# Optimization experiments

Hardware: AMD Instinct MI355X
Metric: run time of the kernel (lower is better)

The kernel has to match this reference:

```python
import jax, jax.numpy as jnp
import numpy as np
import math

D_MODEL = 1024
N_HEADS = 16
HEAD_DIM = D_MODEL // N_HEADS

def setup_inputs() -> dict:
    key = jax.random.key(0)
    k1, k2, k3 = jax.random.split(key, 3)
    B, T = 4, 2048
    x = jax.random.normal(k1, (B, T, D_MODEL), dtype=jnp.float32)
    # weights stored as [in, out]; equivalent to torch Linear weight.T
    w_qkv = jax.random.normal(k2, (D_MODEL, 3 * D_MODEL), dtype=jnp.float32) * (1.0 / math.sqrt(D_MODEL))
    w_proj = jax.random.normal(k3, (D_MODEL, D_MODEL), dtype=jnp.float32) * (1.0 / math.sqrt(D_MODEL))
    return {"x": x, "w_qkv": w_qkv, "w_proj": w_proj}

def reference(x, w_qkv, w_proj):
    B, T, C = x.shape
    qkv = x @ w_qkv  # [B,T,3C]
    q, k, v = jnp.split(qkv, 3, axis=-1)
    # [B,T,C] -> [B,H,T,Dh]
    def to_heads(t):
        return t.reshape(B, T, N_HEADS, HEAD_DIM).transpose(0, 2, 1, 3)
    q, k, v = to_heads(q), to_heads(k), to_heads(v)
    scale = 1.0 / math.sqrt(HEAD_DIM)
    att = jnp.einsum('bhqd,bhkd->bhqk', q, k) * scale  # [B,H,T,T]
    causal = jnp.tril(jnp.ones((T, T), dtype=bool))
    att = jnp.where(causal[None, None], att, -jnp.inf)
    att = jax.nn.softmax(att, axis=-1)
    y = jnp.einsum('bhqk,bhkd->bhqd', att, v)  # [B,H,T,Dh]
    y = y.transpose(0, 2, 1, 3).reshape(B, T, C)
    return y @ w_proj
```

## Files before the change

### kernel.cpp

```cpp
#include <hip/hip_runtime.h>
#include <hip/hip_bf16.h>

typedef __bf16 bf16x8 __attribute__((ext_vector_type(8)));
typedef __bf16 bf16x4 __attribute__((ext_vector_type(4)));
typedef float  f32x4  __attribute__((ext_vector_type(4)));

#define MFMA16(a,b,c) __builtin_amdgcn_mfma_f32_16x16x32_bf16((a),(b),(c),0,0,0)

#define T_SEQ 2048
#define CDIM  1024
#define NH    16
#define DH    64
#define C3    3072
#define QKS   2048

#define GLDS(g, l) __builtin_amdgcn_global_load_lds( \
    (const __attribute__((address_space(1))) void*)(g), \
    (__attribute__((address_space(3))) void*)(l), 16, 0, 0)

__global__ void cast_f32_bf16_kernel(const float* __restrict__ in,
                                     __bf16* __restrict__ out, int n4) {
  int i = blockIdx.x * 256 + threadIdx.x;
  if (i >= n4) return;
  f32x4 v = ((const f32x4*)in)[i];
  bf16x4 o;
  o[0] = (__bf16)v[0]; o[1] = (__bf16)v[1];
  o[2] = (__bf16)v[2]; o[3] = (__bf16)v[3];
  ((bf16x4*)out)[i] = o;
}

__global__ void transpose_cast_kernel(const float* __restrict__ W,
                                      __bf16* __restrict__ WT, int R, int C,
                                      float qscale, int qcols) {
  __shared__ float tile[32][33];
  int c0 = blockIdx.x * 32, r0 = blockIdx.y * 32;
  int tx = threadIdx.x, ty = threadIdx.y;
#pragma unroll
  for (int i = 0; i < 32; i += 8)
    tile[ty + i][tx] = W[(size_t)(r0 + ty + i) * C + c0 + tx];
  __syncthreads();
#pragma unroll
  for (int i = 0; i < 32; i += 8) {
    int c = c0 + ty + i;
    float sc = (c < qcols) ? qscale : 1.0f;
    WT[(size_t)c * R + r0 + tx] = (__bf16)(tile[tx][ty + i] * sc);
  }
}

template <int MODE>
__global__ __launch_bounds__(512, 1)
void gemm256_kernel(const __bf16* __restrict__ A, const __bf16* __restrict__ BT,
                    void* __restrict__ Cout, __bf16* __restrict__ VTp,
                    int K, int nbn) {
  __shared__ __align__(16) __bf16 S[2][2][2][128 * 64];
  const int tid  = threadIdx.x;
  const int lane = tid & 63;
  const int g    = lane >> 4;
  const int l16  = lane & 15;
  const int wave = tid >> 6;
  const int wm   = wave >> 2;
  const int wn   = wave & 3;

  const int nwg = gridDim.x;
  const int sb  = (blockIdx.x & 7) * (nwg >> 3) + (blockIdx.x >> 3);
  const int bn  = sb % nbn;
  const int bm  = sb / nbn;

  const int srow = tid >> 3;
  const int scol = ((tid & 7) << 4) ^ ((srow & 7) << 4);
  const int swz  = (l16 & 7) << 4;

  const __bf16* Abase = A  + (size_t)(bm * 256 + srow) * K + (scol >> 1);
  const __bf16* Bbase = BT + (size_t)(bn * 256 + srow) * K + (scol >> 1);

  f32x4  acc[8][4] = {};
  bf16x8 ar[4][2];
  bf16x8 br[2][2][2];

#define STAGE(BUF, H, K0) do { \
    const __bf16* sp_ = ((H) < 2 ? Abase : Bbase) + (size_t)((H) & 1) * 128 * K + (K0); \
    char* dp_ = (char*)&S[BUF][(H) >> 1][(H) & 1][0] + tid * 16; \
    GLDS(sp_, dp_); \
    GLDS(sp_ + (size_t)64 * K, dp_ + 8192); \
  } while (0)

#define LDA(BUF, MH) do { \
    const char* ab_ = (const char*)&S[BUF][0][wm][0]; \
    _Pragma("unroll") for (int i_ = 0; i_ < 4; ++i_) { \
      const char* rp_ = ab_ + ((MH) * 64 + i_ * 16 + l16) * 128; \
      _Pragma("unroll") for (int kk_ = 0; kk_ < 2; ++kk_) \
        ar[i_][kk_] = *(const bf16x8*)(rp_ + ((kk_ * 64 + g * 16) ^ swz)); \
    } \
  } while (0)

#define LDB(BUF, NHF) do { \
    const char* bb_ = (const char*)&S[BUF][1][wn >> 1][0]; \
    _Pragma("unroll") for (int j_ = 0; j_ < 2; ++j_) { \
      const char* rp_ = bb_ + ((wn & 1) * 64 + ((NHF) * 2 + j_) * 16 + l16) * 128; \
      _Pragma("unroll") for (int kk_ = 0; kk_ < 2; ++kk_) \
        br[NHF][j_][kk_] = *(const bf16x8*)(rp_ + ((kk_ * 64 + g * 16) ^ swz)); \
    } \
  } while (0)

#define MQUAD(MH, NHF) do { \
    __builtin_amdgcn_s_setprio(1); \
    _Pragma("unroll") for (int i_ = 0; i_ < 4; ++i_) \
      _Pragma("unroll") for (int j_ = 0; j_ < 2; ++j_) \
        _Pragma("unroll") for (int kk_ = 0; kk_ < 2; ++kk_) \
          acc[(MH) * 4 + i_][(NHF) * 2 + j_] = \
              MFMA16(ar[i_][kk_], br[NHF][j_][kk_], acc[(MH) * 4 + i_][(NHF) * 2 + j_]); \
    __builtin_amdgcn_s_setprio(0); \
  } while (0)

#define SBAR do { \
    __builtin_amdgcn_sched_barrier(0); \
    __builtin_amdgcn_s_barrier(); \
    __builtin_amdgcn_sched_barrier(0); \
  } while (0)

  STAGE(0, 0, 0); STAGE(0, 1, 0); STAGE(0, 2, 0); STAGE(0, 3, 0);
  STAGE(1, 0, 64);
  asm volatile("s_waitcnt vmcnt(2)" ::: "memory");
  SBAR;

  const int NIT = K >> 7;
#pragma unroll 1
  for (int it = 0; it < NIT; ++it) {
    const int k1 = (2 * it + 1) << 6;
    const int k2 = (2 * it + 2) << 6;
    const int k3 = (2 * it + 3) << 6;
    const bool stg = (it + 1) < NIT;

    LDA(0, 0); LDB(0, 0);
    STAGE(1, 1, k1);
    SBAR; MQUAD(0, 0); SBAR;
    LDB(0, 1);
    STAGE(1, 2, k1);
    SBAR; MQUAD(0, 1); SBAR;
    LDA(0, 1);
    STAGE(1, 3, k1);
    SBAR; MQUAD(1, 1); SBAR;
    if (stg) { STAGE(0, 0, k2); asm volatile("s_waitcnt vmcnt(2)" ::: "memory"); }
    else     { asm volatile("s_waitcnt vmcnt(0)" ::: "memory"); }
    SBAR; MQUAD(1, 0); SBAR;

    LDA(1, 0); LDB(1, 0);
    if (stg) STAGE(0, 1, k2);
    SBAR; MQUAD(0, 0); SBAR;
    LDB(1, 1);
    if (stg) STAGE(0, 2, k2);
    SBAR; MQUAD(0, 1); SBAR;
    LDA(1, 1);
    if (stg) STAGE(0, 3, k2);
    SBAR; MQUAD(1, 1); SBAR;
    if (stg) { STAGE(1, 0, k3); asm volatile("s_waitcnt vmcnt(2)" ::: "memory"); }
    SBAR; MQUAD(1, 0); SBAR;
  }

  if (MODE == 0) {
#pragma unroll
    for (int ii = 0; ii < 8; ++ii) {
      const int row0 = bm * 256 + wm * 128 + ii * 16 + g * 4;
#pragma unroll
      for (int jj = 0; jj < 4; ++jj) {
        const int col = bn * 256 + wn * 64 + jj * 16 + l16;
#pragma unroll
        for (int r = 0; r < 4; ++r)
          ((float*)Cout)[(size_t)(row0 + r) * 1024 + col] = acc[ii][jj][r];
      }
    }
  } else if (bn < 8) {
#pragma unroll
    for (int ii = 0; ii < 8; ++ii) {
      const int row0 = bm * 256 + wm * 128 + ii * 16 + g * 4;
#pragma unroll
      for (int jj = 0; jj < 4; ++jj) {
        const int col = bn * 256 + wn * 64 + jj * 16 + l16;
#pragma unroll
        for (int r = 0; r < 4; ++r)
          ((__bf16*)Cout)[(size_t)(row0 + r) * QKS + col] = (__bf16)acc[ii][jj][r];
      }
    }
  } else {
#pragma unroll
    for (int ii = 0; ii < 8; ++ii) {
      const int row0 = bm * 256 + wm * 128 + ii * 16 + g * 4;
      const int b    = row0 >> 11;
      const int t0   = row0 & 2047;
#pragma unroll
      for (int jj = 0; jj < 4; ++jj) {
        const int c = (bn - 8) * 256 + wn * 64 + jj * 16 + l16;
        bf16x4 pb;
#pragma unroll
        for (int r = 0; r < 4; ++r) pb[r] = (__bf16)acc[ii][jj][r];
        *(bf16x4*)(VTp + ((size_t)((b << 10) + c)) * T_SEQ + t0) = pb;
      }
    }
  }
#undef STAGE
#undef LDA
#undef LDB
#undef MQUAD
#undef SBAR
}

__global__ __launch_bounds__(256)
void attn_kernel(const __bf16* __restrict__ qk, const __bf16* __restrict__ VT,
                 __bf16* __restrict__ y) {
  __shared__ __align__(16) __bf16 Klds[2][64 * 64];
  __shared__ __align__(16) __bf16 Vlds[2][64 * 64];
  __shared__ __align__(16) __bf16 Plds[4][32 * 64];
  const int tid  = threadIdx.x;
  const int lane = tid & 63;
  const int g    = lane >> 4;
  const int l16  = lane & 15;
  const int wave = tid >> 6;

  const int pairid = blockIdx.x >> 6;
  const int bh     = blockIdx.x & 63;
  const int h      = bh & (NH - 1);
  const int b      = bh >> 4;

  const __bf16* Qg = qk + (size_t)b * T_SEQ * QKS + h * DH;
  const __bf16* Kg = Qg + 1024;
  const __bf16* Vt = VT + ((size_t)(b << 10) + h * DH) * T_SEQ;

  const int srow = tid >> 3;
  const int scol = ((tid & 7) * 16) ^ ((srow & 7) << 4);
  const int swz  = (l16 & 7) << 4;

  const float NEG = -3.0e38f;

  bf16x8 ones;
#pragma unroll
  for (int j = 0; j < 8; ++j) ones[j] = (__bf16)1.0f;

  char* Pw = (char*)&Plds[wave][0];

#pragma unroll 1
  for (int ph = 0; ph < 2; ++ph) {
    const int qt    = ph ? (15 - pairid) : pairid;
    const int qbase = qt * 128 + wave * 32;

    bf16x8 qf[2][2];
#pragma unroll
    for (int qg = 0; qg < 2; ++qg)
#pragma unroll
      for (int kk = 0; kk < 2; ++kk)
        qf[qg][kk] = *(const bf16x8*)(Qg + (size_t)(qbase + qg * 16 + l16) * QKS + kk * 32 + g * 8);

    f32x4 o[2][4] = {};
    f32x4 o_l[2]  = {};

    const int nkb = 2 * qt + 2;
    {
      const __bf16* ksrc = Kg + (size_t)srow * QKS + (scol >> 1);
      GLDS(ksrc, (char*)&Klds[0][0] + tid * 16);
      GLDS(ksrc + (size_t)32 * QKS, (char*)&Klds[0][0] + 4096 + tid * 16);
      const __bf16* vsrc = Vt + (size_t)srow * T_SEQ + (scol >> 1);
      GLDS(vsrc, (char*)&Vlds[0][0] + tid * 16);
      GLDS(vsrc + (size_t)32 * T_SEQ, (char*)&Vlds[0][0] + 4096 + tid * 16);
    }
    __syncthreads();

    const __bf16* kstage = Kg + (size_t)(64 + srow) * QKS + (scol >> 1);
    const __bf16* vstage = Vt + (size_t)srow * T_SEQ + 64 + (scol >> 1);

#pragma unroll 1
    for (int kb = 0; kb < nkb; ++kb) {
      const int cur = kb & 1;
      if (kb + 1 < nkb) {
        GLDS(kstage, (char*)&Klds[cur ^ 1][0] + tid * 16);
        GLDS(kstage + (size_t)32 * QKS, (char*)&Klds[cur ^ 1][0] + 4096 + tid * 16);
        GLDS(vstage, (char*)&Vlds[cur ^ 1][0] + tid * 16);
        GLDS(vstage + (size_t)32 * T_SEQ, (char*)&Vlds[cur ^ 1][0] + 4096 + tid * 16);
        kstage += (size_t)64 * QKS;
        vstage += 64;
      }

      f32x4 s[2][4] = {};
      const char* Kb = (const char*)&Klds[cur][0];
#pragma unroll
      for (int st = 0; st < 4; ++st) {
        const char* rowp = Kb + (st * 16 + l16) * 128;
#pragma unroll
        for (int kk = 0; kk < 2; ++kk) {
          bf16x8 kf = *(const bf16x8*)(rowp + ((kk * 64 + g * 16) ^ swz));
          s[0][st] = MFMA16(kf, qf[0][kk], s[0][st]);
          s[1][st] = MFMA16(kf, qf[1][kk], s[1][st]);
        }
      }
      if (kb >= 2 * qt) {
        const int kvbase = (kb - 2 * qt) * 64;
#pragma unroll
        for (int qg = 0; qg < 2; ++qg) {
          const int qloc = wave * 32 + qg * 16 + l16;
#pragma unroll
          for (int st = 0; st < 4; ++st)
#pragma unroll
            for (int r = 0; r < 4; ++r)
              if (kvbase + st * 16 + g * 4 + r > qloc) s[qg][st][r] = NEG;
        }
      }
#pragma unroll
      for (int qg = 0; qg < 2; ++qg) {
        char* Pr = Pw + (qg * 16 + l16) * 128;
#pragma unroll
        for (int st = 0; st < 4; ++st) {
          bf16x4 pb;
#pragma unroll
          for (int r = 0; r < 4; ++r)
            pb[r] = (__bf16)__builtin_amdgcn_exp2f(s[qg][st][r]);
          *(bf16x4*)(Pr + ((st * 32 + g * 8) ^ swz)) = pb;
        }
      }

      const char* Vb = (const char*)&Vlds[cur][0];
#pragma unroll
      for (int hf = 0; hf < 2; ++hf) {
        bf16x8 pf0 = *(const bf16x8*)(Pw + (l16)       * 128 + ((hf * 64 + g * 16) ^ swz));
        bf16x8 pf1 = *(const bf16x8*)(Pw + (16 + l16)  * 128 + ((hf * 64 + g * 16) ^ swz));
        o_l[0] = MFMA16(ones, pf0, o_l[0]);
        o_l[1] = MFMA16(ones, pf1, o_l[1]);
#pragma unroll
        for (int dt = 0; dt < 4; ++dt) {
          bf16x8 vf = *(const bf16x8*)(Vb + (dt * 16 + l16) * 128 + ((hf * 64 + g * 16) ^ swz));
          o[0][dt] = MFMA16(vf, pf0, o[0][dt]);
          o[1][dt] = MFMA16(vf, pf1, o[1][dt]);
        }
      }
      __syncthreads();
    }

#pragma unroll
    for (int qg = 0; qg < 2; ++qg) {
      const float inv_l = 1.0f / o_l[qg][0];
      const int qrow = qbase + qg * 16 + l16;
#pragma unroll
      for (int dt = 0; dt < 4; ++dt)
#pragma unroll
        for (int r = 0; r < 4; ++r)
          y[((size_t)b * T_SEQ + qrow) * CDIM + h * DH + dt * 16 + g * 4 + r] =
              (__bf16)(o[qg][dt][r] * inv_l);
    }
  }
}

extern "C" void kernel_launch(void* const* d_in, const int* in_sizes, int n_in,
                              void* d_out, int out_size, void* d_ws, size_t ws_size,
                              hipStream_t stream) {
  const float* x      = (const float*)d_in[0];
  const float* w_qkv  = (const float*)d_in[1];
  const float* w_proj = (const float*)d_in[2];
  float* out = (float*)d_out;

  __bf16* xb     = (__bf16*)d_ws;
  __bf16* wqkvT  = xb + 8388608;
  __bf16* wprojT = wqkvT + 3145728;
  __bf16* qk     = wprojT + 1048576;
  __bf16* VT     = qk + 16777216;
  __bf16* yb     = VT + 8388608;

  const float SCF = 0.125f * 1.44269504088896340736f;

  cast_f32_bf16_kernel<<<8192, 256, 0, stream>>>(x, xb, 2097152);
  transpose_cast_kernel<<<dim3(96, 32), dim3(32, 8), 0, stream>>>(w_qkv, wqkvT, 1024, 3072, SCF, 1024);
  transpose_cast_kernel<<<dim3(32, 32), dim3(32, 8), 0, stream>>>(w_proj, wprojT, 1024, 1024, 1.0f, 0);
  gemm256_kernel<1><<<384, 512, 0, stream>>>(xb, wqkvT, (void*)qk, VT, 1024, 12);
  attn_kernel<<<512, 256, 0, stream>>>(qk, VT, yb);
  gemm256_kernel<0><<<128, 512, 0, stream>>>(yb, wprojT, (void*)out, nullptr, 1024, 4);
}
```

Measured before the change: 174.6 us.

## Merge GEMM main loop into two MFMA phases per K-tile with paired staging

Restructures the GEMM K-loop schedule so each 64-wide K sub-tile is processed in two larger MFMA phases (both N halves at once) instead of four quadrants. Global-to-LDS staging is issued in pairs, and the vmcnt waits are adjusted to match. The goal is to halve the number of barriers per iteration and give each MFMA burst more work to hide LDS and global latency. The cost is higher register pressure from holding both B halves, and less fine-grained interleaving of loads with compute.

```diff
diff --git a/kernel.cpp b/kernel.cpp
--- a/kernel.cpp
+++ b/kernel.cpp
@@ -102,13 +102,14 @@
     } \
   } while (0)
 
-#define MQUAD(MH, NHF) do { \
+#define MQUAD2(MH) do { \
     __builtin_amdgcn_s_setprio(1); \
-    _Pragma("unroll") for (int i_ = 0; i_ < 4; ++i_) \
-      _Pragma("unroll") for (int j_ = 0; j_ < 2; ++j_) \
-        _Pragma("unroll") for (int kk_ = 0; kk_ < 2; ++kk_) \
-          acc[(MH) * 4 + i_][(NHF) * 2 + j_] = \
-              MFMA16(ar[i_][kk_], br[NHF][j_][kk_], acc[(MH) * 4 + i_][(NHF) * 2 + j_]); \
+    _Pragma("unroll") for (int n_ = 0; n_ < 2; ++n_) \
+      _Pragma("unroll") for (int i_ = 0; i_ < 4; ++i_) \
+        _Pragma("unroll") for (int j_ = 0; j_ < 2; ++j_) \
+          _Pragma("unroll") for (int kk_ = 0; kk_ < 2; ++kk_) \
+            acc[(MH) * 4 + i_][n_ * 2 + j_] = \
+                MFMA16(ar[i_][kk_], br[n_][j_][kk_], acc[(MH) * 4 + i_][n_ * 2 + j_]); \
     __builtin_amdgcn_s_setprio(0); \
   } while (0)
 
@@ -119,8 +120,8 @@
   } while (0)
 
   STAGE(0, 0, 0); STAGE(0, 1, 0); STAGE(0, 2, 0); STAGE(0, 3, 0);
-  STAGE(1, 0, 64);
-  asm volatile("s_waitcnt vmcnt(2)" ::: "memory");
+  STAGE(1, 0, 64); STAGE(1, 2, 64);
+  asm volatile("s_waitcnt vmcnt(4)" ::: "memory");
   SBAR;
 
   const int NIT = K >> 7;
@@ -131,30 +132,29 @@
     const int k3 = (2 * it + 3) << 6;
     const bool stg = (it + 1) < NIT;
 
-    LDA(0, 0); LDB(0, 0);
-    STAGE(1, 1, k1);
-    SBAR; MQUAD(0, 0); SBAR;
-    LDB(0, 1);
-    STAGE(1, 2, k1);
-    SBAR; MQUAD(0, 1); SBAR;
+    LDA(0, 0); LDB(0, 0); LDB(0, 1);
+    STAGE(1, 3, k1); STAGE(1, 1, k1);
+    SBAR; MQUAD2(0); SBAR;
+
     LDA(0, 1);
-    STAGE(1, 3, k1);
-    SBAR; MQUAD(1, 1); SBAR;
-    if (stg) { STAGE(0, 0, k2); asm volatile("s_waitcnt vmcnt(2)" ::: "memory"); }
-    else     { asm volatile("s_waitcnt vmcnt(0)" ::: "memory"); }
-    SBAR; MQUAD(1, 0); SBAR;
-
-    LDA(1, 0); LDB(1, 0);
-    if (stg) STAGE(0, 1, k2);
-    SBAR; MQUAD(0, 0); SBAR;
-    LDB(1, 1);
-    if (stg) STAGE(0, 2, k2);
-    SBAR; MQUAD(0, 1); SBAR;
+    if (stg) {
+      STAGE(0, 0, k2); STAGE(0, 2, k2);
+      asm volatile("s_waitcnt vmcnt(4)" ::: "memory");
+    } else {
+      asm volatile("s_waitcnt vmcnt(0)" ::: "memory");
+    }
+    SBAR; MQUAD2(1); SBAR;
+
+    LDA(1, 0); LDB(1, 0); LDB(1, 1);
+    if (stg) { STAGE(0, 3, k2); STAGE(0, 1, k2); }
+    SBAR; MQUAD2(0); SBAR;
+
     LDA(1, 1);
-    if (stg) STAGE(0, 3, k2);
-    SBAR; MQUAD(1, 1); SBAR;
-    if (stg) { STAGE(1, 0, k3); asm volatile("s_waitcnt vmcnt(2)" ::: "memory"); }
-    SBAR; MQUAD(1, 0); SBAR;
+    if (stg) {
+      STAGE(1, 0, k3); STAGE(1, 2, k3);
+      asm volatile("s_waitcnt vmcnt(4)" ::: "memory");
+    }
+    SBAR; MQUAD2(1); SBAR;
   }
 
   if (MODE == 0) {
@@ -200,7 +200,7 @@
 #undef STAGE
 #undef LDA
 #undef LDB
-#undef MQUAD
+#undef MQUAD2
 #undef SBAR
 }
 
```

Result: no change. 173.8 us (-0.5%).
